# Kernel tuning notes

Measured on AMD Instinct MI355X. Metric: run time of the kernel, lower is better.

The kernel has to match this reference:

```python
import jax, jax.numpy as jnp
import numpy as np

FEAT_DIM = 128
QUANT_BITS = 2
CODE_BIT = 2
CODE_RANGE = 2 ** CODE_BIT            # 4
N_E = (FEAT_DIM * QUANT_BITS) // CODE_BIT   # 128
EMBED_DIM = N_E * CODE_RANGE          # 512
INTER_DIM = min(4096, EMBED_DIM)      # 512
EPS = 1e-6
LN_EPS = 1e-5
B, S = 8, 8192


def setup_inputs() -> dict:
    key = jax.random.key(0)
    ks = jax.random.split(key, 9)
    x = jax.random.normal(ks[0], (B, S, FEAT_DIM), dtype=jnp.float32)
    # uniform noise for gumbel-softmax (transformed to gumbel inside reference)
    gumbel_u = jax.random.uniform(ks[1], (B, S, N_E, CODE_RANGE), dtype=jnp.float32,
                                  minval=1e-9, maxval=1.0)
    # learned parameters (torch default inits approximated)
    embedding = jax.random.normal(ks[2], (N_E * CODE_BIT, FEAT_DIM), dtype=jnp.float32)
    ln_w = jnp.ones((FEAT_DIM,), jnp.float32)
    ln_b = jnp.zeros((FEAT_DIM,), jnp.float32)
    lim1 = 1.0 / np.sqrt(FEAT_DIM)
    w1 = jax.random.uniform(ks[3], (INTER_DIM, FEAT_DIM), jnp.float32, -lim1, lim1)
    b1 = jax.random.uniform(ks[4], (INTER_DIM,), jnp.float32, -lim1, lim1)
    lim2 = 1.0 / np.sqrt(INTER_DIM)
    w2 = jax.random.uniform(ks[5], (EMBED_DIM, INTER_DIM), jnp.float32, -lim2, lim2)
    b2 = jax.random.uniform(ks[6], (EMBED_DIM,), jnp.float32, -lim2, lim2)
    scale = jnp.ones((FEAT_DIM,), jnp.float32)  # learnable_scale (frozen)
    return {"x": x, "gumbel_u": gumbel_u, "ln_w": ln_w, "ln_b": ln_b,
            "w1": w1, "b1": b1, "w2": w2, "b2": b2,
            "embedding": embedding, "scale": scale}


def _forward(x, gumbel_u, ln_w, ln_b, w1, b1, w2, b2, embedding, scale):
    # ---- encode ----
    x = x / (scale + EPS)
    prescale = jnp.linalg.norm(x, axis=-1, keepdims=True)  # [B,S,1]
    x = x / (prescale + EPS)
    mu = jnp.mean(x, axis=-1, keepdims=True)
    var = jnp.mean(jnp.square(x - mu), axis=-1, keepdims=True)
    x = (x - mu) * jax.lax.rsqrt(var + LN_EPS) * ln_w + ln_b
    h = jax.nn.gelu(jnp.einsum('bsf,if->bsi', x, w1) + b1, approximate=False)
    logits = jnp.einsum('bsi,ei->bse', h, w2) + b2          # [B,S,EMBED_DIM]
    # ---- quantize (gumbel-softmax, tau=1, hard, straight-through) ----
    logits = logits.reshape(B, S, N_E, CODE_RANGE)
    g = -jnp.log(-jnp.log(gumbel_u))
    y = jax.nn.softmax(logits + g, axis=-1)
    hard = jax.nn.one_hot(jnp.argmax(y, axis=-1), CODE_RANGE, dtype=y.dtype)
    code4 = hard + y - jax.lax.stop_gradient(y)             # [B,S,N_E,4]
    code2 = code4[..., :2] + code4[..., 2:3]                # fold class-2 into both bits
    code = code2.reshape(B, S, N_E * CODE_BIT)              # [B,S,256] binary
    # ---- decode ----
    rec = jnp.einsum('bsc,cf->bsf', code, embedding)        # [B,S,FEAT_DIM]
    postscale = jnp.linalg.norm(rec, axis=-1, keepdims=True)
    rec = rec / (postscale + EPS) * (prescale + EPS) * (scale + EPS)
    return rec


def reference(x, gumbel_u, ln_w, ln_b, w1, b1, w2, b2, embedding, scale):
    return _forward(x, gumbel_u, ln_w, ln_b, w1, b1, w2, b2, embedding, scale)
```

## Files before the change

kernel.cpp:

```cpp
#include <hip/hip_runtime.h>
#include <math.h>

#define FEAT  128
#define INTER 512
#define EMB   512
#define TB    32

typedef short s16x8 __attribute__((ext_vector_type(8)));
typedef float f32x4 __attribute__((ext_vector_type(4)));

static constexpr float F_EPS    = 1e-6f;
static constexpr float F_LN_EPS = 1e-5f;

#define MFMA(a,b,c) __builtin_amdgcn_mfma_f32_16x16x32_bf16(a,b,c,0,0,0)

#define W1BASE 0
#define W2BASE 196608
#define EBASE  983040

__device__ __forceinline__ unsigned short f2bf(float f) {
    union { float f; unsigned u; } v; v.f = f;
    unsigned r = v.u + 0x7FFFu + ((v.u >> 16) & 1u);
    return (unsigned short)(r >> 16);
}
__device__ __forceinline__ float bf2f(unsigned short h) {
    union { unsigned u; float f; } v; v.u = ((unsigned)h) << 16;
    return v.f;
}
__device__ __forceinline__ void split3(float x, unsigned short& h,
                                       unsigned short& m, unsigned short& l) {
    h = f2bf(x);
    float r1 = x - bf2f(h);
    m = f2bf(r1);
    l = f2bf(r1 - bf2f(m));
}
__device__ __forceinline__ float gelu_exact(float v) {
    return 0.5f * v * (1.0f + erff(v * 0.70710678118654752440f));
}

__global__ __launch_bounds__(256) void vc_pack(const float* __restrict__ w1,
                                               const float* __restrict__ w2,
                                               const float* __restrict__ emb,
                                               unsigned short* __restrict__ P) {
    int id = blockIdx.x * 256 + threadIdx.x;
    int fid = id >> 6, l = id & 63;
    if (fid >= 704) return;
    int lr = l & 15, lq = l >> 4;
    float v[8];
    size_t dst;
    int three = 1;
    if (fid < 128) {
        int kt = fid >> 5, nt = fid & 31;
        const float* s = w1 + (size_t)(nt * 16 + lr) * FEAT + kt * 32 + 8 * lq;
        #pragma unroll
        for (int i = 0; i < 8; ++i) v[i] = s[i];
        dst = W1BASE + (size_t)fid * 1536;
    } else if (fid < 640) {
        int f2 = fid - 128, kt = f2 >> 5, nt = f2 & 31;
        const float* s = w2 + (size_t)(nt * 16 + lr) * INTER + kt * 32 + 8 * lq;
        #pragma unroll
        for (int i = 0; i < 8; ++i) v[i] = s[i];
        dst = W2BASE + (size_t)f2 * 1536;
    } else {
        int f3 = fid - 640, kt = f3 >> 3, nt = f3 & 7;
        #pragma unroll
        for (int i = 0; i < 8; ++i)
            v[i] = emb[(size_t)(kt * 32 + 8 * lq + i) * FEAT + nt * 16 + lr];
        dst = EBASE + (size_t)f3 * 1024;
        three = 0;
    }
    s16x8 vh, vm, vl;
    #pragma unroll
    for (int i = 0; i < 8; ++i) {
        unsigned short a, b, c;
        split3(v[i], a, b, c);
        vh[i] = (short)a; vm[i] = (short)b; vl[i] = (short)c;
    }
    *(s16x8*)(P + dst + l * 8)       = vh;
    *(s16x8*)(P + dst + 512 + l * 8) = vm;
    if (three) *(s16x8*)(P + dst + 1024 + l * 8) = vl;
}

__global__ __launch_bounds__(1024, 8) void vc_fused(
    const float* __restrict__ x,   const float* __restrict__ gu,
    const float* __restrict__ lnw, const float* __restrict__ lnb,
    const float* __restrict__ b1,  const float* __restrict__ b2,
    const float* __restrict__ scl, const unsigned short* __restrict__ wsP,
    float* __restrict__ out)
{
    __shared__ __align__(16) unsigned char smem[79104];
    unsigned short* sXn = (unsigned short*)smem;
    unsigned short* sH  = (unsigned short*)(smem + 24576);
    unsigned*       sC  = (unsigned*)(smem + 73728);
    float*          sPre  = (float*)(smem + 77824);
    float*          sPart = (float*)(smem + 77952);
    float*          sFac  = (float*)(smem + 78976);

    const int tid = threadIdx.x;
    const int w  = tid >> 6;
    const int l  = tid & 63;
    const int lr = l & 15, lq = l >> 4;
    const long tok0 = (long)blockIdx.x * TB;

    if (tid < 512) {
        const int t = tid >> 4;
        const int q = tid & 15;
        const float* xr = x + (tok0 + t) * FEAT + q * 8;
        float v[8];
        #pragma unroll
        for (int k = 0; k < 8; ++k) v[k] = xr[k] / (scl[q * 8 + k] + F_EPS);
        float ss = 0.f;
        #pragma unroll
        for (int k = 0; k < 8; ++k) ss += v[k] * v[k];
        ss += __shfl_xor(ss, 1); ss += __shfl_xor(ss, 2);
        ss += __shfl_xor(ss, 4); ss += __shfl_xor(ss, 8);
        const float pre = sqrtf(ss);
        if (q == 0) sPre[t] = pre;
        const float ip = 1.0f / (pre + F_EPS);
        #pragma unroll
        for (int k = 0; k < 8; ++k) v[k] *= ip;
        float sm = 0.f;
        #pragma unroll
        for (int k = 0; k < 8; ++k) sm += v[k];
        sm += __shfl_xor(sm, 1); sm += __shfl_xor(sm, 2);
        sm += __shfl_xor(sm, 4); sm += __shfl_xor(sm, 8);
        const float mu = sm * (1.0f / 128.0f);
        float vv = 0.f;
        #pragma unroll
        for (int k = 0; k < 8; ++k) { float d = v[k] - mu; vv += d * d; }
        vv += __shfl_xor(vv, 1); vv += __shfl_xor(vv, 2);
        vv += __shfl_xor(vv, 4); vv += __shfl_xor(vv, 8);
        const float rst = 1.0f / sqrtf(vv * (1.0f / 128.0f) + F_LN_EPS);

        const int mt  = t >> 4;
        const int kt  = q >> 2;
        const int sub = q & 3;
        const size_t base = ((size_t)(mt * 4 + kt) * 64 + (t & 15) + 16 * sub) * 8;
        s16x8 vh, vm, vlo;
        #pragma unroll
        for (int i = 0; i < 8; ++i) {
            const float xnv = (v[i] - mu) * rst * lnw[q * 8 + i] + lnb[q * 8 + i];
            unsigned short a, b, c;
            split3(xnv, a, b, c);
            vh[i] = (short)a; vm[i] = (short)b; vlo[i] = (short)c;
        }
        *(s16x8*)(sXn + base)        = vh;
        *(s16x8*)(sXn + 4096 + base) = vm;
        *(s16x8*)(sXn + 8192 + base) = vlo;
    }
    __syncthreads();

    f32x4 acc2[2][2];
    #pragma unroll
    for (int m = 0; m < 2; ++m)
        #pragma unroll
        for (int n = 0; n < 2; ++n)
            #pragma unroll
            for (int r = 0; r < 4; ++r) acc2[m][n][r] = 0.f;

    for (int half = 0; half < 2; ++half) {
        f32x4 acc1[2];
        #pragma unroll
        for (int m = 0; m < 2; ++m)
            #pragma unroll
            for (int r = 0; r < 4; ++r) acc1[m][r] = 0.f;

        #pragma unroll
        for (int kt = 0; kt < 4; ++kt) {
            const int nt = half * 16 + w;
            const unsigned short* bp =
                wsP + W1BASE + (size_t)(kt * 32 + nt) * 1536 + l * 8;
            #pragma unroll
            for (int m = 0; m < 2; ++m) {
                const size_t base = ((size_t)(m * 4 + kt) * 64 + l) * 8;
                const s16x8 A0 = *(const s16x8*)(sXn + base);
                const s16x8 A1 = *(const s16x8*)(sXn + 4096 + base);
                const s16x8 A2 = *(const s16x8*)(sXn + 8192 + base);
                f32x4 c = acc1[m];
                {
                    const s16x8 bl = *(const s16x8*)(bp + 1024);
                    c = MFMA(A0, bl, c);
                }
                {
                    const s16x8 bm = *(const s16x8*)(bp + 512);
                    c = MFMA(A1, bm, c);
                    c = MFMA(A0, bm, c);
                }
                {
                    const s16x8 bh = *(const s16x8*)bp;
                    c = MFMA(A2, bh, c);
                    c = MFMA(A1, bh, c);
                    c = MFMA(A0, bh, c);
                }
                acc1[m] = c;
            }
        }

        {
            const float b1v = b1[half * 256 + w * 16 + lr];
            #pragma unroll
            for (int m = 0; m < 2; ++m)
                #pragma unroll
                for (int r = 0; r < 4; ++r) {
                    const float h = gelu_exact(acc1[m][r] + b1v);
                    unsigned short hh, hm, hl;
                    split3(h, hh, hm, hl);
                    const int tokr = 4 * lq + r;
                    const int row  = m * 16 + tokr;
                    const int nl   = w * 16 + lr;
                    const int gsw  = (nl >> 3) ^ (tokr & 7);
                    const size_t off = (size_t)row * 256 + gsw * 8 + (nl & 7);
                    sH[off]          = hh;
                    sH[8192 + off]   = hm;
                    sH[16384 + off]  = hl;
                }
        }
        __syncthreads();

        for (int kk = 0; kk < 8; ++kk) {
            s16x8 A0[2], A1[2], A2[2];
            #pragma unroll
            for (int m = 0; m < 2; ++m) {
                const int row = m * 16 + lr;
                const int gsw = (kk * 4 + lq) ^ (lr & 7);
                const size_t off = (size_t)row * 256 + (size_t)gsw * 8;
                A0[m] = *(const s16x8*)(sH + off);
                A1[m] = *(const s16x8*)(sH + 8192 + off);
                A2[m] = *(const s16x8*)(sH + 16384 + off);
            }
            #pragma unroll
            for (int ntl = 0; ntl < 2; ++ntl) {
                const int fid2 = (half * 8 + kk) * 32 + (w * 2 + ntl);
                const unsigned short* bp =
                    wsP + W2BASE + (size_t)fid2 * 1536 + l * 8;
                {
                    const s16x8 bl = *(const s16x8*)(bp + 1024);
                    acc2[0][ntl] = MFMA(A0[0], bl, acc2[0][ntl]);
                    acc2[1][ntl] = MFMA(A0[1], bl, acc2[1][ntl]);
                }
                {
                    const s16x8 bm = *(const s16x8*)(bp + 512);
                    acc2[0][ntl] = MFMA(A1[0], bm, acc2[0][ntl]);
                    acc2[1][ntl] = MFMA(A1[1], bm, acc2[1][ntl]);
                    acc2[0][ntl] = MFMA(A0[0], bm, acc2[0][ntl]);
                    acc2[1][ntl] = MFMA(A0[1], bm, acc2[1][ntl]);
                }
                {
                    const s16x8 bh = *(const s16x8*)bp;
                    acc2[0][ntl] = MFMA(A2[0], bh, acc2[0][ntl]);
                    acc2[1][ntl] = MFMA(A2[1], bh, acc2[1][ntl]);
                    acc2[0][ntl] = MFMA(A1[0], bh, acc2[0][ntl]);
                    acc2[1][ntl] = MFMA(A1[1], bh, acc2[1][ntl]);
                    acc2[0][ntl] = MFMA(A0[0], bh, acc2[0][ntl]);
                    acc2[1][ntl] = MFMA(A0[1], bh, acc2[1][ntl]);
                }
            }
        }
        __syncthreads();
    }

    {
        float b2v[2];
        #pragma unroll
        for (int ntl = 0; ntl < 2; ++ntl) b2v[ntl] = b2[w * 32 + ntl * 16 + lr];
        const int qq  = lr >> 2;
        const int cls = l & 3;
        #pragma unroll
        for (int m = 0; m < 2; ++m)
            #pragma unroll
            for (int ntl = 0; ntl < 2; ++ntl) {
                #pragma unroll
                for (int r = 0; r < 4; ++r) {
                    const long tg = tok0 + m * 16 + 4 * lq + r;
                    const float u = gu[tg * 512 + w * 32 + ntl * 16 + lr];
                    float v = acc2[m][ntl][r] + b2v[ntl] - logf(-logf(u));
                    int   ci = cls;
                    float v1 = __shfl_xor(v, 1); int c1 = __shfl_xor(ci, 1);
                    if (v1 > v || (v1 == v && c1 < ci)) { v = v1; ci = c1; }
                    float v2 = __shfl_xor(v, 2); int c2 = __shfl_xor(ci, 2);
                    if (v2 > v || (v2 == v && c2 < ci)) { v = v2; ci = c2; }
                    if (cls == 0) {
                        const int row = m * 16 + 4 * lq + r;
                        const int col = (w * 2 + ntl) ^ ((row & 7) << 2);
                        ((unsigned char*)(sC + row * 32 + col))[qq] = (unsigned char)ci;
                    }
                }
            }
    }
    __syncthreads();

    const int nt_d = w & 7;
    const int mp   = w >> 3;
    f32x4 accd;
    #pragma unroll
    for (int r = 0; r < 4; ++r) accd[r] = 0.f;

    #pragma unroll
    for (int kt = 0; kt < 8; ++kt) {
        const unsigned short* bp = wsP + EBASE + (size_t)(kt * 8 + nt_d) * 1024 + l * 8;
        const int row = mp * 16 + lr;
        const int col = (kt * 4 + lq) ^ ((row & 7) << 2);
        const unsigned cw = sC[row * 32 + col];
        s16x8 a;
        #pragma unroll
        for (int q2 = 0; q2 < 4; ++q2) {
            const unsigned c = (cw >> (8 * q2)) & 0xffu;
            a[2 * q2]     = ((c & 1u) == 0u) ? (short)0x3F80 : (short)0;
            a[2 * q2 + 1] = (((c + 1u) & 2u) != 0u) ? (short)0x3F80 : (short)0;
        }
        {
            const s16x8 bh = *(const s16x8*)bp;
            accd = MFMA(a, bh, accd);
        }
        {
            const s16x8 bl = *(const s16x8*)(bp + 512);
            accd = MFMA(a, bl, accd);
        }
    }
    __syncthreads();

    {
        float ps[4];
        #pragma unroll
        for (int r = 0; r < 4; ++r) {
            float s = accd[r] * accd[r];
            s += __shfl_xor(s, 1); s += __shfl_xor(s, 2);
            s += __shfl_xor(s, 4); s += __shfl_xor(s, 8);
            ps[r] = s;
        }
        if (lr == 0)
            *(float4*)(sPart + nt_d * 32 + mp * 16 + 4 * lq) =
                make_float4(ps[0], ps[1], ps[2], ps[3]);
    }
    __syncthreads();
    if (tid < 32) {
        float ssum = 0.f;
        #pragma unroll
        for (int g = 0; g < 8; ++g) ssum += sPart[g * 32 + tid];
        const float post = sqrtf(ssum);
        sFac[tid] = (1.0f / (post + F_EPS)) * (sPre[tid] + F_EPS);
    }
    __syncthreads();
    {
        const float sclv = scl[nt_d * 16 + lr] + F_EPS;
        #pragma unroll
        for (int r = 0; r < 4; ++r) {
            const int tokr = mp * 16 + 4 * lq + r;
            const float o = accd[r] * sFac[tokr] * sclv;
            out[(tok0 + tokr) * FEAT + nt_d * 16 + lr] = o;
        }
    }
}

extern "C" void kernel_launch(void* const* d_in, const int* in_sizes, int n_in,
                              void* d_out, int out_size, void* d_ws, size_t ws_size,
                              hipStream_t stream) {
    const float* x   = (const float*)d_in[0];
    const float* gu  = (const float*)d_in[1];
    const float* lnw = (const float*)d_in[2];
    const float* lnb = (const float*)d_in[3];
    const float* w1  = (const float*)d_in[4];
    const float* b1  = (const float*)d_in[5];
    const float* w2  = (const float*)d_in[6];
    const float* b2  = (const float*)d_in[7];
    const float* emb = (const float*)d_in[8];
    const float* scl = (const float*)d_in[9];
    float* out = (float*)d_out;

    unsigned short* wsP = (unsigned short*)d_ws;

    hipLaunchKernelGGL(vc_pack, dim3(176), dim3(256), 0, stream, w1, w2, emb, wsP);

    const int ntok = in_sizes[0] / FEAT;
    hipLaunchKernelGGL(vc_fused, dim3(ntok / TB), dim3(1024), 0, stream,
                       x, gu, lnw, lnb, b1, b2, scl, wsP, out);
}
```

Baseline: 343.9 us.

## Halve block to 512 threads, chunk hidden layer into quarters, alias LDS

The fused kernel now runs 8 waves per block instead of 16. Each wave covers twice as many output tiles in the second GEMM and decode stages, and the hidden layer is processed in four chunks of 128 rather than two of 256. The code-byte buffer reuses the normalized-input region of shared memory, cutting LDS per block from about 79KB to about 50KB so more blocks can be resident per CU. In exchange each wave holds more accumulators, raising register pressure, and there are more barrier phases per block.

```diff
diff --git a/kernel.cpp b/kernel.cpp
--- a/kernel.cpp
+++ b/kernel.cpp
@@ -81,20 +81,20 @@
     if (three) *(s16x8*)(P + dst + 1024 + l * 8) = vl;
 }
 
-__global__ __launch_bounds__(1024, 8) void vc_fused(
+__global__ __launch_bounds__(512, 6) void vc_fused(
     const float* __restrict__ x,   const float* __restrict__ gu,
     const float* __restrict__ lnw, const float* __restrict__ lnb,
     const float* __restrict__ b1,  const float* __restrict__ b2,
     const float* __restrict__ scl, const unsigned short* __restrict__ wsP,
     float* __restrict__ out)
 {
-    __shared__ __align__(16) unsigned char smem[79104];
+    __shared__ __align__(16) unsigned char smem[50432];
     unsigned short* sXn = (unsigned short*)smem;
+    unsigned*       sC  = (unsigned*)smem;
     unsigned short* sH  = (unsigned short*)(smem + 24576);
-    unsigned*       sC  = (unsigned*)(smem + 73728);
-    float*          sPre  = (float*)(smem + 77824);
-    float*          sPart = (float*)(smem + 77952);
-    float*          sFac  = (float*)(smem + 78976);
+    float*          sPre  = (float*)(smem + 49152);
+    float*          sPart = (float*)(smem + 49280);
+    float*          sFac  = (float*)(smem + 50304);
 
     const int tid = threadIdx.x;
     const int w  = tid >> 6;
@@ -102,7 +102,7 @@
     const int lr = l & 15, lq = l >> 4;
     const long tok0 = (long)blockIdx.x * TB;
 
-    if (tid < 512) {
+    {
         const int t = tid >> 4;
         const int q = tid & 15;
         const float* xr = x + (tok0 + t) * FEAT + q * 8;
@@ -150,15 +150,15 @@
     }
     __syncthreads();
 
-    f32x4 acc2[2][2];
+    f32x4 acc2[2][4];
     #pragma unroll
     for (int m = 0; m < 2; ++m)
         #pragma unroll
-        for (int n = 0; n < 2; ++n)
+        for (int n = 0; n < 4; ++n)
             #pragma unroll
             for (int r = 0; r < 4; ++r) acc2[m][n][r] = 0.f;
 
-    for (int half = 0; half < 2; ++half) {
+    for (int qtr = 0; qtr < 4; ++qtr) {
         f32x4 acc1[2];
         #pragma unroll
         for (int m = 0; m < 2; ++m)
@@ -167,7 +167,7 @@
 
         #pragma unroll
         for (int kt = 0; kt < 4; ++kt) {
-            const int nt = half * 16 + w;
+            const int nt = qtr * 8 + w;
             const unsigned short* bp =
                 wsP + W1BASE + (size_t)(kt * 32 + nt) * 1536 + l * 8;
             #pragma unroll
@@ -197,7 +197,7 @@
         }
 
         {
-            const float b1v = b1[half * 256 + w * 16 + lr];
+            const float b1v = b1[qtr * 128 + w * 16 + lr];
             #pragma unroll
             for (int m = 0; m < 2; ++m)
                 #pragma unroll
@@ -209,28 +209,29 @@
                     const int row  = m * 16 + tokr;
                     const int nl   = w * 16 + lr;
                     const int gsw  = (nl >> 3) ^ (tokr & 7);
-                    const size_t off = (size_t)row * 256 + gsw * 8 + (nl & 7);
+                    const size_t off = (size_t)row * 128 + gsw * 8 + (nl & 7);
                     sH[off]          = hh;
-                    sH[8192 + off]   = hm;
-                    sH[16384 + off]  = hl;
+                    sH[4096 + off]   = hm;
+                    sH[8192 + off]   = hl;
                 }
         }
         __syncthreads();
 
-        for (int kk = 0; kk < 8; ++kk) {
+        #pragma unroll
+        for (int kk = 0; kk < 4; ++kk) {
             s16x8 A0[2], A1[2], A2[2];
             #pragma unroll
             for (int m = 0; m < 2; ++m) {
                 const int row = m * 16 + lr;
                 const int gsw = (kk * 4 + lq) ^ (lr & 7);
-                const size_t off = (size_t)row * 256 + (size_t)gsw * 8;
+                const size_t off = (size_t)row * 128 + (size_t)gsw * 8;
                 A0[m] = *(const s16x8*)(sH + off);
-                A1[m] = *(const s16x8*)(sH + 8192 + off);
-                A2[m] = *(const s16x8*)(sH + 16384 + off);
-            }
-            #pragma unroll
-            for (int ntl = 0; ntl < 2; ++ntl) {
-                const int fid2 = (half * 8 + kk) * 32 + (w * 2 + ntl);
+                A1[m] = *(const s16x8*)(sH + 4096 + off);
+                A2[m] = *(const s16x8*)(sH + 8192 + off);
+            }
+            #pragma unroll
+            for (int ntl = 0; ntl < 4; ++ntl) {
+                const int fid2 = (qtr * 4 + kk) * 32 + (w * 4 + ntl);
                 const unsigned short* bp =
                     wsP + W2BASE + (size_t)fid2 * 1536 + l * 8;
                 {
@@ -260,20 +261,18 @@
     }
 
     {
-        float b2v[2];
-        #pragma unroll
-        for (int ntl = 0; ntl < 2; ++ntl) b2v[ntl] = b2[w * 32 + ntl * 16 + lr];
         const int qq  = lr >> 2;
         const int cls = l & 3;
         #pragma unroll
         for (int m = 0; m < 2; ++m)
             #pragma unroll
-            for (int ntl = 0; ntl < 2; ++ntl) {
+            for (int ntl = 0; ntl < 4; ++ntl) {
+                const float b2v = b2[w * 64 + ntl * 16 + lr];
                 #pragma unroll
                 for (int r = 0; r < 4; ++r) {
                     const long tg = tok0 + m * 16 + 4 * lq + r;
-                    const float u = gu[tg * 512 + w * 32 + ntl * 16 + lr];
-                    float v = acc2[m][ntl][r] + b2v[ntl] - logf(-logf(u));
+                    const float u = gu[tg * 512 + w * 64 + ntl * 16 + lr];
+                    float v = acc2[m][ntl][r] + b2v - logf(-logf(u));
                     int   ci = cls;
                     float v1 = __shfl_xor(v, 1); int c1 = __shfl_xor(ci, 1);
                     if (v1 > v || (v1 == v && c1 < ci)) { v = v1; ci = c1; }
@@ -281,7 +280,7 @@
                     if (v2 > v || (v2 == v && c2 < ci)) { v = v2; ci = c2; }
                     if (cls == 0) {
                         const int row = m * 16 + 4 * lq + r;
-                        const int col = (w * 2 + ntl) ^ ((row & 7) << 2);
+                        const int col = (w * 4 + ntl) ^ ((row & 7) << 2);
                         ((unsigned char*)(sC + row * 32 + col))[qq] = (unsigned char)ci;
                     }
                 }
@@ -289,48 +288,50 @@
     }
     __syncthreads();
 
-    const int nt_d = w & 7;
-    const int mp   = w >> 3;
-    f32x4 accd;
+    f32x4 accd[2];
     #pragma unroll
-    for (int r = 0; r < 4; ++r) accd[r] = 0.f;
+    for (int mi = 0; mi < 2; ++mi)
+        #pragma unroll
+        for (int r = 0; r < 4; ++r) accd[mi][r] = 0.f;
 
     #pragma unroll
     for (int kt = 0; kt < 8; ++kt) {
-        const unsigned short* bp = wsP + EBASE + (size_t)(kt * 8 + nt_d) * 1024 + l * 8;
-        const int row = mp * 16 + lr;
-        const int col = (kt * 4 + lq) ^ ((row & 7) << 2);
-        const unsigned cw = sC[row * 32 + col];
-        s16x8 a;
-        #pragma unroll
-        for (int q2 = 0; q2 < 4; ++q2) {
-            const unsigned c = (cw >> (8 * q2)) & 0xffu;
-            a[2 * q2]     = ((c & 1u) == 0u) ? (short)0x3F80 : (short)0;
-            a[2 * q2 + 1] = (((c + 1u) & 2u) != 0u) ? (short)0x3F80 : (short)0;
-        }
-        {
-            const s16x8 bh = *(const s16x8*)bp;
-            accd = MFMA(a, bh, accd);
-        }
-        {
-            const s16x8 bl = *(const s16x8*)(bp + 512);
-            accd = MFMA(a, bl, accd);
+        const unsigned short* bp = wsP + EBASE + (size_t)(kt * 8 + w) * 1024 + l * 8;
+        const s16x8 bh = *(const s16x8*)bp;
+        const s16x8 bl = *(const s16x8*)(bp + 512);
+        #pragma unroll
+        for (int mi = 0; mi < 2; ++mi) {
+            const int row = mi * 16 + lr;
+            const int col = (kt * 4 + lq) ^ ((row & 7) << 2);
+            const unsigned cw = sC[row * 32 + col];
+            s16x8 a;
+            #pragma unroll
+            for (int q2 = 0; q2 < 4; ++q2) {
+                const unsigned c = (cw >> (8 * q2)) & 0xffu;
+                a[2 * q2]     = ((c & 1u) == 0u) ? (short)0x3F80 : (short)0;
+                a[2 * q2 + 1] = (((c + 1u) & 2u) != 0u) ? (short)0x3F80 : (short)0;
+            }
+            accd[mi] = MFMA(a, bh, accd[mi]);
+            accd[mi] = MFMA(a, bl, accd[mi]);
         }
     }
     __syncthreads();
 
     {
-        float ps[4];
-        #pragma unroll
-        for (int r = 0; r < 4; ++r) {
-            float s = accd[r] * accd[r];
-            s += __shfl_xor(s, 1); s += __shfl_xor(s, 2);
-            s += __shfl_xor(s, 4); s += __shfl_xor(s, 8);
-            ps[r] = s;
-        }
-        if (lr == 0)
-            *(float4*)(sPart + nt_d * 32 + mp * 16 + 4 * lq) =
-                make_float4(ps[0], ps[1], ps[2], ps[3]);
+        #pragma unroll
+        for (int mi = 0; mi < 2; ++mi) {
+            float ps[4];
+            #pragma unroll
+            for (int r = 0; r < 4; ++r) {
+                float s = accd[mi][r] * accd[mi][r];
+                s += __shfl_xor(s, 1); s += __shfl_xor(s, 2);
+                s += __shfl_xor(s, 4); s += __shfl_xor(s, 8);
+                ps[r] = s;
+            }
+            if (lr == 0)
+                *(float4*)(sPart + w * 32 + mi * 16 + 4 * lq) =
+                    make_float4(ps[0], ps[1], ps[2], ps[3]);
+        }
     }
     __syncthreads();
     if (tid < 32) {
@@ -342,13 +343,15 @@
     }
     __syncthreads();
     {
-        const float sclv = scl[nt_d * 16 + lr] + F_EPS;
-        #pragma unroll
-        for (int r = 0; r < 4; ++r) {
-            const int tokr = mp * 16 + 4 * lq + r;
-            const float o = accd[r] * sFac[tokr] * sclv;
-            out[(tok0 + tokr) * FEAT + nt_d * 16 + lr] = o;
-        }
+        const float sclv = scl[w * 16 + lr] + F_EPS;
+        #pragma unroll
+        for (int mi = 0; mi < 2; ++mi)
+            #pragma unroll
+            for (int r = 0; r < 4; ++r) {
+                const int tokr = mi * 16 + 4 * lq + r;
+                const float o = accd[mi][r] * sFac[tokr] * sclv;
+                out[(tok0 + tokr) * FEAT + w * 16 + lr] = o;
+            }
     }
 }
 
@@ -372,6 +375,6 @@
     hipLaunchKernelGGL(vc_pack, dim3(176), dim3(256), 0, stream, w1, w2, emb, wsP);
 
     const int ntok = in_sizes[0] / FEAT;
-    hipLaunchKernelGGL(vc_fused, dim3(ntok / TB), dim3(1024), 0, stream,
+    hipLaunchKernelGGL(vc_fused, dim3(ntok / TB), dim3(512), 0, stream,
                        x, gu, lnw, lnb, b1, b2, scl, wsP, out);
 }
```

Measured after the change: 346.8 us. No clear change (+0.8%).
